# Kernel optimization log

Hardware: AMD Instinct MI355X
Metric: run time of the kernel (lower is better)

## Reference

```python
import jax, jax.numpy as jnp
import numpy as np

B, S, D, H = 4, 4096, 1024, 128

def setup_inputs() -> dict:
    key = jax.random.key(0)
    k1, k2, k3, k4 = jax.random.split(key, 4)
    scale = 1.0 / np.sqrt(D)
    return {
        "x": jax.random.normal(k1, (B, S, D), dtype=jnp.float32),
        "Wq": jax.random.normal(k2, (H, D), dtype=jnp.float32) * scale,
        "Wk": jax.random.normal(k3, (H, D), dtype=jnp.float32) * scale,
        "Wv": jax.random.normal(k4, (H, D), dtype=jnp.float32) * scale,
    }

def reference(x, Wq, Wk, Wv):
    # Linear(in,out,bias=False): y = x @ W.T
    q = jnp.einsum('bsd,hd->bsh', x, Wq)
    k = jnp.einsum('bsd,hd->bsh', x, Wk)
    v = jnp.einsum('bsd,hd->bsh', x, Wv)
    scores = jnp.einsum('bqh,bkh->bqk', q, k) / jnp.sqrt(jnp.float32(H))
    num_toks = x.shape[1]
    causal = jnp.tril(jnp.ones((num_toks, num_toks), dtype=bool))
    scores = jnp.where(causal[None, :, :], scores, -jnp.inf)
    probs = jax.nn.softmax(scores, axis=-1)
    return jnp.einsum('bqk,bkh->bqh', probs, v)
```

## Files before the change

### kernel.cpp

```cpp
#include <hip/hip_runtime.h>
#include <hip/hip_bf16.h>

#define BATCH  4
#define SEQ    4096
#define DMODEL 1024
#define HDIM   128
#define MROWS  (BATCH * SEQ)
#define NT32   (SEQ / 32)
#define T32    (BATCH * NT32)
#define NS     4

#define BM 64
#define BN 96
#define BK 64
#define KT (DMODEL / BK)

typedef __attribute__((ext_vector_type(8)))  short short8;
typedef __attribute__((ext_vector_type(4)))  float floatx4;
typedef __attribute__((ext_vector_type(16))) float floatx16;
typedef unsigned int u32;

static __device__ __forceinline__ short f2bf(float f) {
    __hip_bfloat16 h = __float2bfloat16(f);
    union { __hip_bfloat16 h; short s; } u; u.h = h;
    return u.s;
}

static __device__ __forceinline__ float bf2f(unsigned short s) {
    union { u32 u; float f; } v; v.u = ((u32)s) << 16;
    return v.f;
}

static __device__ __forceinline__ short8 ld8(const unsigned short* p) {
    return *reinterpret_cast<const short8*>(p);
}

static __device__ __forceinline__ void gload_lds16(const void* g, void* l) {
    __builtin_amdgcn_global_load_lds(
        (const __attribute__((address_space(1))) unsigned int*)g,
        (__attribute__((address_space(3))) unsigned int*)l,
        16, 0, 0);
}

static __device__ __forceinline__ u32 cvtpk_bf16(float a, float b) {
    u32 r;
    asm("v_cvt_pk_bf16_f32 %0, %1, %2" : "=v"(r) : "v"(a), "v"(b));
    return r;
}

static __device__ __forceinline__ void swap_halves(u32& a, u32& b) {
#if __has_builtin(__builtin_amdgcn_permlane32_swap)
    typedef __attribute__((ext_vector_type(2))) int int2v;
    int2v r = __builtin_amdgcn_permlane32_swap((int)a, (int)b, false, false);
    a = (u32)r[0]; b = (u32)r[1];
#else
    u32 ap = (u32)__shfl_xor((int)a, 32);
    u32 bp = (u32)__shfl_xor((int)b, 32);
    const bool hih = (threadIdx.x & 32) != 0;
    u32 na = hih ? bp : a;
    u32 nb = hih ? b : ap;
    a = na; b = nb;
#endif
}


__global__ __launch_bounds__(256) void cvt_w_kernel(
    const float* __restrict__ Wq, const float* __restrict__ Wk,
    const float* __restrict__ Wv, unsigned short* __restrict__ wbf)
{
    const int n8w = HDIM * DMODEL / 8;
    int i = blockIdx.x * 256 + threadIdx.x;
    if (i >= 3 * n8w) return;
    const int which = i / n8w;
    const int j = i - which * n8w;
    const float* src = (which == 0) ? Wq : (which == 1) ? Wk : Wv;
    const float scale = (which == 0) ? 0.08838834764831845f : 1.0f;
    const float4* s4 = reinterpret_cast<const float4*>(src);
    float4 a = s4[2 * j];
    float4 b = s4[2 * j + 1];
    short8 o;
    o[0] = f2bf(a.x * scale); o[1] = f2bf(a.y * scale);
    o[2] = f2bf(a.z * scale); o[3] = f2bf(a.w * scale);
    o[4] = f2bf(b.x * scale); o[5] = f2bf(b.y * scale);
    o[6] = f2bf(b.z * scale); o[7] = f2bf(b.w * scale);
    reinterpret_cast<short8*>(wbf)[i] = o;
}

__global__ __launch_bounds__(256, 4) void qkv_kernel(
    const float* __restrict__ x,
    const unsigned short* __restrict__ wbf,
    unsigned short* __restrict__ qt,
    unsigned short* __restrict__ kt,
    unsigned short* __restrict__ vtl)
{
    __shared__ __align__(16) unsigned short A_lds[2][BM][BK];
    __shared__ __align__(16) unsigned short B_lds[2][BN][BK];

    const int raw  = blockIdx.x;
    const int vid  = (raw & 7) * 128 + (raw >> 3);
    const int mblk = vid >> 2;
    const int nblk = vid & 3;
    const int m0   = mblk * BM;
    const int n0   = nblk * BN;

    const int tid  = threadIdx.x;
    const int wv   = tid >> 6;
    const int lane = tid & 63;
    const int lr   = lane & 15;
    const int lh   = lane >> 4;
    const int wm   = wv >> 1;
    const int wn   = wv & 1;

    const int ar = tid >> 2;
    const int aq = tid & 3;
    const float* asrc = x + (size_t)(m0 + ar) * DMODEL + aq * 16;

    const int brow  = lane >> 3;
    const int bunit = (lane & 7) ^ brow;

    floatx4 acc[2][3];
#pragma unroll
    for (int mf = 0; mf < 2; ++mf)
#pragma unroll
        for (int nf = 0; nf < 3; ++nf) acc[mf][nf] = (floatx4){0.f, 0.f, 0.f, 0.f};

    {
#pragma unroll
        for (int j = 0; j < 3; ++j) {
            const int rbase = (j * 4 + wv) * 8;
            gload_lds16(wbf + (size_t)(n0 + rbase + brow) * DMODEL + bunit * 8,
                        &B_lds[0][rbase][0]);
        }
        float4 f0 = *reinterpret_cast<const float4*>(asrc);
        float4 f1 = *reinterpret_cast<const float4*>(asrc + 4);
        float4 f2 = *reinterpret_cast<const float4*>(asrc + 8);
        float4 f3 = *reinterpret_cast<const float4*>(asrc + 12);
        short8 v0, v1;
        v0[0] = f2bf(f0.x); v0[1] = f2bf(f0.y); v0[2] = f2bf(f0.z); v0[3] = f2bf(f0.w);
        v0[4] = f2bf(f1.x); v0[5] = f2bf(f1.y); v0[6] = f2bf(f1.z); v0[7] = f2bf(f1.w);
        v1[0] = f2bf(f2.x); v1[1] = f2bf(f2.y); v1[2] = f2bf(f2.z); v1[3] = f2bf(f2.w);
        v1[4] = f2bf(f3.x); v1[5] = f2bf(f3.y); v1[6] = f2bf(f3.z); v1[7] = f2bf(f3.w);
        const int u0 = (2 * aq)     ^ (ar & 7);
        const int u1 = (2 * aq + 1) ^ (ar & 7);
        *reinterpret_cast<short8*>(&A_lds[0][ar][u0 * 8]) = v0;
        *reinterpret_cast<short8*>(&A_lds[0][ar][u1 * 8]) = v1;
    }
    __syncthreads();

    for (int ktile = 0; ktile < KT; ++ktile) {
        const int cur = ktile & 1;
        const int nxt = cur ^ 1;
        float4 f0, f1, f2, f3;
        if (ktile + 1 < KT) {
#pragma unroll
            for (int j = 0; j < 3; ++j) {
                const int rbase = (j * 4 + wv) * 8;
                gload_lds16(wbf + (size_t)(n0 + rbase + brow) * DMODEL
                                + (ktile + 1) * BK + bunit * 8,
                            &B_lds[nxt][rbase][0]);
            }
            const float* a = asrc + (ktile + 1) * BK;
            f0 = *reinterpret_cast<const float4*>(a);
            f1 = *reinterpret_cast<const float4*>(a + 4);
            f2 = *reinterpret_cast<const float4*>(a + 8);
            f3 = *reinterpret_cast<const float4*>(a + 12);
        }
#pragma unroll
        for (int kk = 0; kk < 2; ++kk) {
            const int uswz = (kk * 4 + lh) ^ (lr & 7);
            short8 af[2], bfr[3];
#pragma unroll
            for (int mf = 0; mf < 2; ++mf)
                af[mf] = ld8(&A_lds[cur][wm * 32 + mf * 16 + lr][uswz * 8]);
#pragma unroll
            for (int nf = 0; nf < 3; ++nf)
                bfr[nf] = ld8(&B_lds[cur][wn * 48 + nf * 16 + lr][uswz * 8]);
#pragma unroll
            for (int mf = 0; mf < 2; ++mf)
#pragma unroll
                for (int nf = 0; nf < 3; ++nf)
                    acc[mf][nf] = __builtin_amdgcn_mfma_f32_16x16x32_bf16(
                        af[mf], bfr[nf], acc[mf][nf], 0, 0, 0);
        }
        if (ktile + 1 < KT) {
            short8 v0, v1;
            v0[0] = f2bf(f0.x); v0[1] = f2bf(f0.y); v0[2] = f2bf(f0.z); v0[3] = f2bf(f0.w);
            v0[4] = f2bf(f1.x); v0[5] = f2bf(f1.y); v0[6] = f2bf(f1.z); v0[7] = f2bf(f1.w);
            v1[0] = f2bf(f2.x); v1[1] = f2bf(f2.y); v1[2] = f2bf(f2.z); v1[3] = f2bf(f2.w);
            v1[4] = f2bf(f3.x); v1[5] = f2bf(f3.y); v1[6] = f2bf(f3.z); v1[7] = f2bf(f3.w);
            const int u0 = (2 * aq)     ^ (ar & 7);
            const int u1 = (2 * aq + 1) ^ (ar & 7);
            *reinterpret_cast<short8*>(&A_lds[nxt][ar][u0 * 8]) = v0;
            *reinterpret_cast<short8*>(&A_lds[nxt][ar][u1 * 8]) = v1;
        }
        __syncthreads();
    }

    __syncthreads();
    unsigned short* out_l = &A_lds[0][0][0];

    const int t0 = (m0 & (SEQ - 1)) >> 5;
    const int bb = m0 >> 12;
    const int st = wm;

#pragma unroll
    for (int nf = 0; nf < 3; ++nf) {
        const int cl = wn * 48 + nf * 16 + lr;
#pragma unroll
        for (int mf = 0; mf < 2; ++mf) {
#pragma unroll
            for (int r = 0; r < 4; ++r) {
                const int srow = mf * 16 + lh * 4 + r;
                const unsigned short vv = (unsigned short)f2bf(acc[mf][nf][r]);
                int lf, off;
                if (nblk == 0) {
                    lf  = st * 6 + (cl >> 4);
                    off = ((cl >> 3) & 1) * 256 + srow * 8 + (cl & 7);
                } else if (nblk == 1) {
                    lf  = (cl < 32) ? st * 6 + (cl >> 4)
                                    : st * 6 + 2 + ((cl - 32) >> 4);
                    off = ((cl >> 3) & 1) * 256 + srow * 8 + (cl & 7);
                } else if (nblk == 2) {
                    if (cl < 64) {
                        lf  = st * 6 + (cl >> 4);
                        off = ((cl >> 3) & 1) * 256 + srow * 8 + (cl & 7);
                    } else {
                        const int dg = cl - 64;
                        lf  = st * 6 + 4 + ((srow >> 4) & 1);
                        off = ((srow >> 3) & 1) * 256 + dg * 8 + (srow & 7);
                    }
                } else {
                    const int d = cl + 32;
                    lf  = st * 6 + ((d >> 5) - 1) * 2 + ((srow >> 4) & 1);
                    off = ((srow >> 3) & 1) * 256 + (d & 31) * 8 + (srow & 7);
                }
                out_l[lf * 512 + off] = vv;
            }
        }
    }
    __syncthreads();

#pragma unroll
    for (int k = 0; k < 3; ++k) {
        const int u   = tid + 256 * k;
        const int fb  = u >> 6;
        const int iu  = u & 63;
        const int fst = (fb >= 6) ? 1 : 0;
        const int li  = fb - 6 * fst;
        const size_t tb8 = (size_t)((bb * NT32 + t0 + fst) * 8);
        unsigned short* gbase;
        if (nblk == 0) {
            gbase = qt + ((tb8 + li) << 9);
        } else if (nblk == 1) {
            gbase = (li < 2) ? qt  + ((tb8 + 6 + li) << 9)
                             : kt  + ((tb8 + (li - 2)) << 9);
        } else if (nblk == 2) {
            gbase = (li < 4) ? kt  + ((tb8 + 4 + li) << 9)
                             : vtl + ((tb8 + (li - 4)) << 9);
        } else {
            gbase = vtl + ((tb8 + 2 + li) << 9);
        }
        *reinterpret_cast<short8*>(gbase + iu * 8) =
            *reinterpret_cast<const short8*>(&out_l[fb * 512 + iu * 8]);
    }
}

__global__ __launch_bounds__(64) void attn_kernel(
    const unsigned short* __restrict__ qt,
    const unsigned short* __restrict__ kt,
    const unsigned short* __restrict__ vtl,
    unsigned short* __restrict__ pacc,
    float* __restrict__ pm,
    float* __restrict__ pl)
{
    const int bid  = blockIdx.x;
    const int xcd  = bid & 7;
    const int b    = xcd >> 1;
    const int par  = xcd & 1;
    const int idx  = bid >> 3;
    const int s    = idx & 3;
    const int trk  = idx >> 2;
    const int t32b = (NT32 - 1) - (trk * 2 + par);
    const int q0   = t32b * 32;
    const int t32  = b * NT32 + t32b;
    const int lane = threadIdx.x & 63;
    const int l31  = lane & 31;
    const int hih  = lane >> 5;

    const int nkv   = q0 + 32;
    const int chunk = ((nkv + NS * 32 - 1) / (NS * 32)) * 32;
    const int lo    = s * chunk;
    const int hikv  = (lo + chunk < nkv) ? lo + chunk : nkv;
    const size_t mlbase = (size_t)(s * T32 + t32) * 32;

    if (lo >= hikv) {
        if (lane < 32) { pm[mlbase + l31] = -3.0e38f; pl[mlbase + l31] = 0.f; }
        return;
    }

    const unsigned short* qtb =
        qt + ((size_t)((b * NT32 + t32b) * 8) << 9) + lane * 8;
    short8 qa[8];
#pragma unroll
    for (int ks = 0; ks < 8; ++ks) qa[ks] = ld8(qtb + (ks << 9));

    const unsigned short* ktbase = kt  + ((size_t)(b * NT32 * 8) << 9) + lane * 8;
    const unsigned short* vtbase = vtl + ((size_t)(b * NT32 * 8) << 9) + lane * 8;

    floatx16 acco[4];
#pragma unroll
    for (int db = 0; db < 4; ++db)
#pragma unroll
        for (int i = 0; i < 16; ++i) acco[db][i] = 0.f;
    float m_r = -3.0e38f, l_r = 0.f;

    short8 kf[8];
#pragma unroll
    for (int ks = 0; ks < 8; ++ks)
        kf[ks] = ld8(ktbase + ((size_t)((lo >> 5) * 8 + ks) << 9));

    for (int kv0 = lo; kv0 < hikv; kv0 += 32) {
        const int t = kv0 >> 5;
        const unsigned short* vtb = vtbase + ((size_t)(t * 8) << 9);

        short8 vf[8];
#pragma unroll
        for (int j = 0; j < 8; ++j) vf[j] = ld8(vtb + (j << 9));

        floatx16 sc;
#pragma unroll
        for (int i = 0; i < 16; ++i) sc[i] = 0.f;
        __builtin_amdgcn_s_setprio(1);
#pragma unroll
        for (int ks = 0; ks < 8; ++ks)
            sc = __builtin_amdgcn_mfma_f32_32x32x16_bf16(kf[ks], qa[ks], sc, 0, 0, 0);
        __builtin_amdgcn_s_setprio(0);

        const int tn = (kv0 + 32 < hikv) ? t + 1 : t;
#pragma unroll
        for (int ks = 0; ks < 8; ++ks)
            kf[ks] = ld8(ktbase + ((size_t)(tn * 8 + ks) << 9));

        if (kv0 == q0) {
#pragma unroll
            for (int r = 0; r < 16; ++r) {
                const int kvloc = (r & 3) + 8 * (r >> 2) + 4 * hih;
                if (kvloc > l31) sc[r] = -3.0e38f;
            }
        }
        float t8[8];
#pragma unroll
        for (int i = 0; i < 8; ++i) t8[i] = fmaxf(sc[i], sc[i + 8]);
        float t4a = fmaxf(t8[0], t8[4]), t4b = fmaxf(t8[1], t8[5]);
        float t4c = fmaxf(t8[2], t8[6]), t4d = fmaxf(t8[3], t8[7]);
        float pmax = fmaxf(fmaxf(t4a, t4b), fmaxf(t4c, t4d));
        pmax = fmaxf(pmax, __shfl_xor(pmax, 32));
        if (__any(pmax > m_r + 8.f)) {
            const float mn  = fmaxf(m_r, pmax);
            const float fac = __expf(m_r - mn);
            m_r = mn; l_r *= fac;
#pragma unroll
            for (int db = 0; db < 4; ++db)
#pragma unroll
                for (int i = 0; i < 16; ++i) acco[db][i] *= fac;
        }
        float p[16];
#pragma unroll
        for (int r = 0; r < 16; ++r) p[r] = __expf(sc[r] - m_r);
        float s8[8];
#pragma unroll
        for (int i = 0; i < 8; ++i) s8[i] = p[i] + p[i + 8];
        float s4a = s8[0] + s8[4], s4b = s8[1] + s8[5];
        float s4c = s8[2] + s8[6], s4d = s8[3] + s8[7];
        float ps = (s4a + s4b) + (s4c + s4d);
        ps += __shfl_xor(ps, 32);
        l_r += ps;
        u32 pk0 = cvtpk_bf16(p[0], p[1]),   pk2 = cvtpk_bf16(p[4], p[5]);
        swap_halves(pk0, pk2);
        u32 pk1 = cvtpk_bf16(p[2], p[3]),   pk3 = cvtpk_bf16(p[6], p[7]);
        swap_halves(pk1, pk3);
        u32 pk4 = cvtpk_bf16(p[8], p[9]),   pk6 = cvtpk_bf16(p[12], p[13]);
        swap_halves(pk4, pk6);
        u32 pk5 = cvtpk_bf16(p[10], p[11]), pk7 = cvtpk_bf16(p[14], p[15]);
        swap_halves(pk5, pk7);
        union { u32 u[4]; short8 s8v; } ua, ub;
        ua.u[0] = pk0; ua.u[1] = pk1; ua.u[2] = pk2; ua.u[3] = pk3;
        ub.u[0] = pk4; ub.u[1] = pk5; ub.u[2] = pk6; ub.u[3] = pk7;
        const short8 pa0 = ua.s8v, pa1 = ub.s8v;
        __builtin_amdgcn_s_setprio(1);
#pragma unroll
        for (int db = 0; db < 4; ++db) {
            acco[db] = __builtin_amdgcn_mfma_f32_32x32x16_bf16(vf[2 * db],     pa0, acco[db], 0, 0, 0);
            acco[db] = __builtin_amdgcn_mfma_f32_32x32x16_bf16(vf[2 * db + 1], pa1, acco[db], 0, 0, 0);
        }
        __builtin_amdgcn_s_setprio(0);
    }

    unsigned short* pt = pacc + (size_t)(s * T32 + t32) * 128 * 32;
#pragma unroll
    for (int db = 0; db < 4; ++db)
#pragma unroll
        for (int r = 0; r < 16; ++r) {
            const int dloc = db * 32 + (r & 3) + 8 * (r >> 2) + 4 * hih;
            pt[(size_t)dloc * 32 + l31] = (unsigned short)f2bf(acco[db][r]);
        }
    if (lane < 32) { pm[mlbase + l31] = m_r; pl[mlbase + l31] = l_r; }
}

__global__ __launch_bounds__(256) void combine_kernel(
    const unsigned short* __restrict__ pacc, const float* __restrict__ pm,
    const float* __restrict__ pl, float* __restrict__ out)
{
    __shared__ float wlds[NS][32];
    __shared__ float tlds[128][33];
    const int t32 = blockIdx.x;
    const int tid = threadIdx.x;

    if (tid < 32) {
        const int q = tid;
        float ms[NS], ls[NS];
        float M = -3.0e38f;
#pragma unroll
        for (int s = 0; s < NS; ++s) {
            ms[s] = pm[(size_t)(s * T32 + t32) * 32 + q];
            ls[s] = pl[(size_t)(s * T32 + t32) * 32 + q];
            M = fmaxf(M, ms[s]);
        }
        float w[NS], den = 0.f;
#pragma unroll
        for (int s = 0; s < NS; ++s) { w[s] = __expf(ms[s] - M); den += w[s] * ls[s]; }
        const float inv = 1.f / den;
#pragma unroll
        for (int s = 0; s < NS; ++s) wlds[s][q] = w[s] * inv;
    }
    __syncthreads();

#pragma unroll
    for (int rep = 0; rep < 16; ++rep) {
        const int flat = rep * 256 + tid;
        const int d = flat >> 5, q = flat & 31;
        float acc = 0.f;
#pragma unroll
        for (int s = 0; s < NS; ++s)
            acc += wlds[s][q] *
                   bf2f(pacc[((size_t)(s * T32 + t32) * 128 + d) * 32 + q]);
        tlds[d][q] = acc;
    }
    __syncthreads();

    const size_t row0 = (size_t)t32 * 32;
#pragma unroll
    for (int rep = 0; rep < 16; ++rep) {
        const int flat = rep * 256 + tid;
        const int q = flat >> 7, d = flat & 127;
        out[(row0 + q) * 128 + d] = tlds[d][q];
    }
}

extern "C" void kernel_launch(void* const* d_in, const int* in_sizes, int n_in,
                              void* d_out, int out_size, void* d_ws, size_t ws_size,
                              hipStream_t stream)
{
    const float* x  = (const float*)d_in[0];
    const float* Wq = (const float*)d_in[1];
    const float* Wk = (const float*)d_in[2];
    const float* Wv = (const float*)d_in[3];
    float* out = (float*)d_out;

    const size_t TBUF = (size_t)BATCH * NT32 * 8 * 512;

    unsigned short* wbf  = (unsigned short*)d_ws;
    unsigned short* qt   = wbf + (size_t)384 * DMODEL;
    unsigned short* ktb  = qt + TBUF;
    unsigned short* vtl  = ktb + TBUF;
    unsigned short* pacc = vtl + TBUF;
    float* pm = (float*)(pacc + (size_t)NS * T32 * 128 * 32);
    float* pl = pm + (size_t)NS * T32 * 32;

    const int n8w3 = 3 * HDIM * DMODEL / 8;
    cvt_w_kernel<<<(n8w3 + 255) / 256, 256, 0, stream>>>(Wq, Wk, Wv, wbf);

    qkv_kernel<<<(MROWS / BM) * (384 / BN), 256, 0, stream>>>(x, wbf, qt, ktb, vtl);

    attn_kernel<<<T32 * NS, 64, 0, stream>>>(qt, ktb, vtl, pacc, pm, pl);

    combine_kernel<<<T32, 256, 0, stream>>>(pacc, pm, pl, out);
}
```

Before: 79.66 us.

## Pre-tile weights into MFMA fragment order and load B operands directly from global

The weight conversion kernel now writes bf16 weights in a tiled layout where each 16x32 block matches the MFMA B-fragment lane order. The QKV GEMM drops the B shared-memory buffer and its async global-to-LDS copies, and each lane loads its 16-byte fragment straight from global/L2. This halves LDS usage and removes LDS traffic for weights, which may raise occupancy. In exchange, every wave rereads weights from cache with no prefetch or double buffering, so the MFMA loop may stall on global load latency.

```diff
diff --git a/kernel.cpp b/kernel.cpp
--- a/kernel.cpp
+++ b/kernel.cpp
@@ -33,13 +33,6 @@
 
 static __device__ __forceinline__ short8 ld8(const unsigned short* p) {
     return *reinterpret_cast<const short8*>(p);
-}
-
-static __device__ __forceinline__ void gload_lds16(const void* g, void* l) {
-    __builtin_amdgcn_global_load_lds(
-        (const __attribute__((address_space(1))) unsigned int*)g,
-        (__attribute__((address_space(3))) unsigned int*)l,
-        16, 0, 0);
 }
 
 static __device__ __forceinline__ u32 cvtpk_bf16(float a, float b) {
@@ -66,7 +59,7 @@
 
 __global__ __launch_bounds__(256) void cvt_w_kernel(
     const float* __restrict__ Wq, const float* __restrict__ Wk,
-    const float* __restrict__ Wv, unsigned short* __restrict__ wbf)
+    const float* __restrict__ Wv, unsigned short* __restrict__ wbt)
 {
     const int n8w = HDIM * DMODEL / 8;
     int i = blockIdx.x * 256 + threadIdx.x;
@@ -83,18 +76,22 @@
     o[2] = f2bf(a.z * scale); o[3] = f2bf(a.w * scale);
     o[4] = f2bf(b.x * scale); o[5] = f2bf(b.y * scale);
     o[6] = f2bf(b.z * scale); o[7] = f2bf(b.w * scale);
-    reinterpret_cast<short8*>(wbf)[i] = o;
+    const int n  = which * HDIM + (j >> 7);
+    const int k0 = (j & 127) * 8;
+    const size_t addr =
+        ((size_t)((n >> 4) * 32 + (k0 >> 5)) << 9)
+        + (((n & 15) + (((k0 >> 3) & 3) * 16)) * 8);
+    *reinterpret_cast<short8*>(wbt + addr) = o;
 }
 
 __global__ __launch_bounds__(256, 4) void qkv_kernel(
     const float* __restrict__ x,
-    const unsigned short* __restrict__ wbf,
+    const unsigned short* __restrict__ wbt,
     unsigned short* __restrict__ qt,
     unsigned short* __restrict__ kt,
     unsigned short* __restrict__ vtl)
 {
     __shared__ __align__(16) unsigned short A_lds[2][BM][BK];
-    __shared__ __align__(16) unsigned short B_lds[2][BN][BK];
 
     const int raw  = blockIdx.x;
     const int vid  = (raw & 7) * 128 + (raw >> 3);
@@ -102,6 +99,7 @@
     const int nblk = vid & 3;
     const int m0   = mblk * BM;
     const int n0   = nblk * BN;
+    const int nb0  = n0 >> 4;
 
     const int tid  = threadIdx.x;
     const int wv   = tid >> 6;
@@ -115,9 +113,6 @@
     const int aq = tid & 3;
     const float* asrc = x + (size_t)(m0 + ar) * DMODEL + aq * 16;
 
-    const int brow  = lane >> 3;
-    const int bunit = (lane & 7) ^ brow;
-
     floatx4 acc[2][3];
 #pragma unroll
     for (int mf = 0; mf < 2; ++mf)
@@ -125,12 +120,6 @@
         for (int nf = 0; nf < 3; ++nf) acc[mf][nf] = (floatx4){0.f, 0.f, 0.f, 0.f};
 
     {
-#pragma unroll
-        for (int j = 0; j < 3; ++j) {
-            const int rbase = (j * 4 + wv) * 8;
-            gload_lds16(wbf + (size_t)(n0 + rbase + brow) * DMODEL + bunit * 8,
-                        &B_lds[0][rbase][0]);
-        }
         float4 f0 = *reinterpret_cast<const float4*>(asrc);
         float4 f1 = *reinterpret_cast<const float4*>(asrc + 4);
         float4 f2 = *reinterpret_cast<const float4*>(asrc + 8);
@@ -152,13 +141,6 @@
         const int nxt = cur ^ 1;
         float4 f0, f1, f2, f3;
         if (ktile + 1 < KT) {
-#pragma unroll
-            for (int j = 0; j < 3; ++j) {
-                const int rbase = (j * 4 + wv) * 8;
-                gload_lds16(wbf + (size_t)(n0 + rbase + brow) * DMODEL
-                                + (ktile + 1) * BK + bunit * 8,
-                            &B_lds[nxt][rbase][0]);
-            }
             const float* a = asrc + (ktile + 1) * BK;
             f0 = *reinterpret_cast<const float4*>(a);
             f1 = *reinterpret_cast<const float4*>(a + 4);
@@ -167,14 +149,17 @@
         }
 #pragma unroll
         for (int kk = 0; kk < 2; ++kk) {
-            const int uswz = (kk * 4 + lh) ^ (lr & 7);
+            const int uswz   = (kk * 4 + lh) ^ (lr & 7);
+            const int kchunk = ktile * 2 + kk;
             short8 af[2], bfr[3];
 #pragma unroll
             for (int mf = 0; mf < 2; ++mf)
                 af[mf] = ld8(&A_lds[cur][wm * 32 + mf * 16 + lr][uswz * 8]);
 #pragma unroll
             for (int nf = 0; nf < 3; ++nf)
-                bfr[nf] = ld8(&B_lds[cur][wn * 48 + nf * 16 + lr][uswz * 8]);
+                bfr[nf] = ld8(wbt
+                    + ((size_t)((nb0 + wn * 3 + nf) * 32 + kchunk) << 9)
+                    + lane * 8);
 #pragma unroll
             for (int mf = 0; mf < 2; ++mf)
 #pragma unroll
@@ -469,8 +454,8 @@
 
     const size_t TBUF = (size_t)BATCH * NT32 * 8 * 512;
 
-    unsigned short* wbf  = (unsigned short*)d_ws;
-    unsigned short* qt   = wbf + (size_t)384 * DMODEL;
+    unsigned short* wbt  = (unsigned short*)d_ws;
+    unsigned short* qt   = wbt + (size_t)384 * DMODEL;
     unsigned short* ktb  = qt + TBUF;
     unsigned short* vtl  = ktb + TBUF;
     unsigned short* pacc = vtl + TBUF;
@@ -478,9 +463,9 @@
     float* pl = pm + (size_t)NS * T32 * 32;
 
     const int n8w3 = 3 * HDIM * DMODEL / 8;
-    cvt_w_kernel<<<(n8w3 + 255) / 256, 256, 0, stream>>>(Wq, Wk, Wv, wbf);
-
-    qkv_kernel<<<(MROWS / BM) * (384 / BN), 256, 0, stream>>>(x, wbf, qt, ktb, vtl);
+    cvt_w_kernel<<<(n8w3 + 255) / 256, 256, 0, stream>>>(Wq, Wk, Wv, wbt);
+
+    qkv_kernel<<<(MROWS / BM) * (384 / BN), 256, 0, stream>>>(x, wbt, qt, ktb, vtl);
 
     attn_kernel<<<T32 * NS, 64, 0, stream>>>(qt, ktb, vtl, pacc, pm, pl);
 
```

Result: no change. 79.08 us (-0.7%).
